# Kernel optimization log

Measured on AMD Instinct MI355X. Metric: run time of the kernel, lower is better.

Reference implementation:

```python
import jax, jax.numpy as jnp
import numpy as np

NUM_BITS = 10
D_MODEL = 256
D_INNER = 512                      # expand=2 * hidden
D_STATE = 64
N_HEADS = 8                        # D_INNER // head_dim(64)
HEAD_DIM = 64
CONV_DIM = D_INNER + 2 * D_STATE   # 640
D_PROJ = D_INNER + CONV_DIM + N_HEADS  # 1160
KERNEL = 4
EPS = 1e-5
N_TOKENS = 16384


def _hilbert_code(coords):
    # coords: (N,3) int32 in [0, 2**NUM_BITS); Skilling's AxesToTranspose + bit interleave
    n = 3
    x = [coords[:, i] for i in range(n)]
    M = 1 << (NUM_BITS - 1)
    Q = M
    while Q > 1:
        P = Q - 1
        for i in range(n):
            cond = (x[i] & Q) > 0
            t = (x[0] ^ x[i]) & P
            x0_new = jnp.where(cond, x[0] ^ P, x[0] ^ t)
            xi_new = jnp.where(cond, x[i], x[i] ^ t)
            x[0] = x0_new
            if i > 0:
                x[i] = xi_new
        Q >>= 1
    for i in range(1, n):
        x[i] = x[i] ^ x[i - 1]
    t = jnp.zeros_like(x[0])
    Q = M
    while Q > 1:
        t = jnp.where((x[n - 1] & Q) > 0, t ^ (Q - 1), t)
        Q >>= 1
    x = [xi ^ t for xi in x]
    code = jnp.zeros_like(x[0])
    for b in range(NUM_BITS - 1, -1, -1):
        for i in range(n):
            code = (code << 1) | ((x[i] >> b) & 1)
    return code


def _serialized_orders(query_pos):
    # quantize to a 2**NUM_BITS grid, Hilbert-encode, sort ('hilbert' and 'hilbert-trans' = x/y swapped)
    pmin = query_pos.min(0)
    pmax = query_pos.max(0)
    g = ((query_pos - pmin) / (pmax - pmin + 1e-6) * (2 ** NUM_BITS - 1))
    g = jnp.clip(g, 0, 2 ** NUM_BITS - 1).astype(jnp.int32)
    orders, inverses = [], []
    for perm in ((0, 1, 2), (1, 0, 2)):
        code = _hilbert_code(g[:, jnp.array(perm)])
        o = jnp.argsort(code)
        orders.append(o)
        inverses.append(jnp.argsort(o))
    return orders, inverses


def _ln(x, w, b):
    m = x.mean(-1, keepdims=True)
    xc = x - m
    return xc * jax.lax.rsqrt(jnp.mean(xc * xc, -1, keepdims=True) + EPS) * w + b


def _mamba2(x, p):
    # x: (B, L, D_MODEL)
    B, L, _ = x.shape
    zxbcdt = x @ p['in_proj']                           # (B,L,1160)
    gate = zxbcdt[..., :D_INNER]
    xBC = zxbcdt[..., D_INNER:D_INNER + CONV_DIM]
    dt = zxbcdt[..., D_INNER + CONV_DIM:]               # (B,L,H)
    # causal depthwise conv over time
    xc = jnp.moveaxis(xBC, -1, 1)                       # (B,C,L)
    xc = jax.lax.conv_general_dilated(
        xc, p['conv_w'][:, None, :], window_strides=(1,),
        padding=[(KERNEL - 1, 0)], dimension_numbers=('NCH', 'OIH', 'NCH'),
        feature_group_count=CONV_DIM)
    xc = xc + p['conv_b'][None, :, None]
    xBC = jax.nn.silu(jnp.moveaxis(xc, 1, -1))          # (B,L,C)
    xs = xBC[..., :D_INNER].reshape(B, L, N_HEADS, HEAD_DIM)
    Bm = xBC[..., D_INNER:D_INNER + D_STATE]            # (B,L,S), n_groups=1 broadcast over heads
    Cm = xBC[..., D_INNER + D_STATE:]                   # (B,L,S)
    dt = jax.nn.softplus(dt + p['dt_bias'])             # (B,L,H)
    A = -jnp.exp(p['A_log'])                            # (H,)
    dA = jnp.exp(dt * A)                                # (B,L,H)

    def step(h, inp):
        dA_t, dt_t, x_t, B_t, C_t = inp                 # (B,H),(B,H),(B,H,P),(B,S),(B,S)
        h = h * dA_t[..., None, None] + (dt_t[..., None] * x_t)[..., None] * B_t[:, None, None, :]
        y = jnp.einsum('bhps,bs->bhp', h, C_t)
        return h, y

    tm = lambda a: jnp.moveaxis(a, 1, 0)
    h0 = jnp.zeros((B, N_HEADS, HEAD_DIM, D_STATE), x.dtype)
    _, ys = jax.lax.scan(step, h0, (tm(dA), tm(dt), tm(xs), tm(Bm), tm(Cm)))
    y = jnp.moveaxis(ys, 0, 1) + p['D'][None, None, :, None] * xs   # (B,L,H,P) + D skip
    y = y.reshape(B, L, D_INNER)
    # gated RMSNorm (MambaRMSNormGated)
    y = y * jax.nn.silu(gate)
    y = y * jax.lax.rsqrt(jnp.mean(y * y, -1, keepdims=True) + EPS) * p['norm_w']
    return y @ p['out_proj']                            # (B,L,D_MODEL)


def _forward(query, query_pos, pre_w, pre_b, fin_w, fin_b, layer_params):
    orders, invs = _serialized_orders(query_pos)
    q = query
    for p in layer_params:
        shortcut = q
        qn = _ln(q, pre_w, pre_b)
        stacked = jnp.stack([qn[orders[0]], qn[orders[1]]])   # (2, N, d) multi-path serialization
        y = _mamba2(stacked, p)
        q = shortcut + (y[0][invs[0]] + y[1][invs[1]]) * 0.5  # scatter back + average paths
        q = _ln(q, fin_w, fin_b)
    return q


def setup_inputs() -> dict:
    key = jax.random.key(0)
    ks = jax.random.split(key, 24)
    inp = {
        'query': jax.random.normal(ks[0], (N_TOKENS, D_MODEL), jnp.float32),
        'query_pos': jax.random.uniform(ks[1], (N_TOKENS, 3), jnp.float32),
        'pre_w': jnp.ones((D_MODEL,), jnp.float32),
        'pre_b': jnp.zeros((D_MODEL,), jnp.float32),
        'fin_w': jnp.ones((D_MODEL,), jnp.float32),
        'fin_b': jnp.zeros((D_MODEL,), jnp.float32),
    }
    for i in range(2):
        k = jax.random.split(ks[2 + i], 6)
        inp[f'in_proj{i}'] = jax.random.normal(k[0], (D_MODEL, D_PROJ), jnp.float32) * 0.02
        inp[f'conv_w{i}'] = jax.random.normal(k[1], (CONV_DIM, KERNEL), jnp.float32) * 0.2
        inp[f'conv_b{i}'] = jnp.zeros((CONV_DIM,), jnp.float32)
        inp[f'dt_bias{i}'] = jax.random.uniform(k[2], (N_HEADS,), jnp.float32, -4.0, -1.0)
        inp[f'A_log{i}'] = jnp.log(jnp.arange(1, N_HEADS + 1, dtype=jnp.float32))
        inp[f'D{i}'] = jnp.ones((N_HEADS,), jnp.float32)
        inp[f'norm_w{i}'] = jnp.ones((D_INNER,), jnp.float32)
        inp[f'out_proj{i}'] = jax.random.normal(k[3], (D_INNER, D_MODEL), jnp.float32) * 0.02
    return inp


def reference(query, query_pos, pre_w, pre_b, fin_w, fin_b,
              in_proj0, conv_w0, conv_b0, dt_bias0, A_log0, D0, norm_w0, out_proj0,
              in_proj1, conv_w1, conv_b1, dt_bias1, A_log1, D1, norm_w1, out_proj1):
    layer_params = [
        dict(in_proj=in_proj0, conv_w=conv_w0, conv_b=conv_b0, dt_bias=dt_bias0,
             A_log=A_log0, D=D0, norm_w=norm_w0, out_proj=out_proj0),
        dict(in_proj=in_proj1, conv_w=conv_w1, conv_b=conv_b1, dt_bias=dt_bias1,
             A_log=A_log1, D=D1, norm_w=norm_w1, out_proj=out_proj1),
    ]
    return _forward(query, query_pos, pre_w, pre_b, fin_w, fin_b, layer_params)
```

## Files before the change

kernel.cpp:

```cpp
#include <hip/hip_runtime.h>
#include <stdint.h>

#define L_TOK 16384
#define DM 256
#define DI 512
#define DS 64
#define NH 8
#define HD 64
#define CD 640
#define DP 1160
#define CHUNK 64
#define NC 256
#define EPSF 1e-5f

typedef __attribute__((ext_vector_type(8))) short short8;
typedef __attribute__((ext_vector_type(4))) float f32x4;

#define GLL16(gp, lp) __builtin_amdgcn_global_load_lds((const __attribute__((address_space(1))) void*)(gp), (__attribute__((address_space(3))) void*)(lp), 16, 0, 0)

__device__ __forceinline__ float warp_sum(float v) {
  v += __shfl_xor(v, 1, 64);
  v += __shfl_xor(v, 2, 64);
  v += __shfl_xor(v, 4, 64);
  v += __shfl_xor(v, 8, 64);
  v += __shfl_xor(v, 16, 64);
  v += __shfl_xor(v, 32, 64);
  return v;
}

__device__ __forceinline__ float fexp(float x) { return __expf(x); }
__device__ __forceinline__ float fsilu(float x) { return x * __builtin_amdgcn_rcpf(1.0f + __expf(-x)); }

__device__ __forceinline__ unsigned short f2bf(float f) {
  unsigned int u = __float_as_uint(f);
  unsigned int r = (u + 0x7FFFu + ((u >> 16) & 1u)) >> 16;
  return (unsigned short)r;
}
__device__ __forceinline__ float bf2f(unsigned short u) {
  return __uint_as_float(((unsigned int)u) << 16);
}


__global__ __launch_bounds__(256) void minmax_part(const float* __restrict__ pos, float* __restrict__ part) {
  __shared__ float sm[6][4];
  int tid = threadIdx.x;
  int t = blockIdx.x*256 + tid;
  float a = pos[t*3+0], b = pos[t*3+1], c = pos[t*3+2];
  float mn0=a, mn1=b, mn2=c, mx0=a, mx1=b, mx2=c;
  #pragma unroll
  for (int d = 1; d < 64; d <<= 1) {
    mn0=fminf(mn0,__shfl_xor(mn0,d,64));
    mn1=fminf(mn1,__shfl_xor(mn1,d,64));
    mn2=fminf(mn2,__shfl_xor(mn2,d,64));
    mx0=fmaxf(mx0,__shfl_xor(mx0,d,64));
    mx1=fmaxf(mx1,__shfl_xor(mx1,d,64));
    mx2=fmaxf(mx2,__shfl_xor(mx2,d,64));
  }
  if ((tid & 63) == 0) {
    int w = tid >> 6;
    sm[0][w]=mn0; sm[1][w]=mn1; sm[2][w]=mn2;
    sm[3][w]=mx0; sm[4][w]=mx1; sm[5][w]=mx2;
  }
  __syncthreads();
  if (tid < 6) {
    float r = sm[tid][0];
    if (tid < 3) { r=fminf(r,sm[tid][1]); r=fminf(r,sm[tid][2]); r=fminf(r,sm[tid][3]); }
    else         { r=fmaxf(r,sm[tid][1]); r=fmaxf(r,sm[tid][2]); r=fmaxf(r,sm[tid][3]); }
    part[blockIdx.x*6 + tid] = r;
  }
}

__device__ unsigned int hilbert3(unsigned int a, unsigned int b, unsigned int c) {
  unsigned int x0 = a, x1 = b, x2 = c;
  for (unsigned int Q = 512u; Q > 1u; Q >>= 1) {
    unsigned int P = Q - 1u;
    { if (x0 & Q) x0 ^= P; }
    {
      unsigned int t = (x0 ^ x1) & P;
      if (x1 & Q) { x0 ^= P; }
      else { x0 ^= t; x1 ^= t; }
    }
    {
      unsigned int t = (x0 ^ x2) & P;
      if (x2 & Q) { x0 ^= P; }
      else { x0 ^= t; x2 ^= t; }
    }
  }
  x1 ^= x0; x2 ^= x1;
  unsigned int tt = 0;
  for (unsigned int Q = 512u; Q > 1u; Q >>= 1)
    if (x2 & Q) tt ^= (Q - 1u);
  x0 ^= tt; x1 ^= tt; x2 ^= tt;
  unsigned int code = 0;
  #pragma unroll
  for (int bb = 9; bb >= 0; --bb) {
    code = (code << 1) | ((x0 >> bb) & 1u);
    code = (code << 1) | ((x1 >> bb) & 1u);
    code = (code << 1) | ((x2 >> bb) & 1u);
  }
  return code;
}

__global__ __launch_bounds__(256) void hilbert_kernel(const float* __restrict__ pos, const float* __restrict__ part,
                                                      unsigned long long* __restrict__ keys) {
  __shared__ float spmm[6];
  int tid = threadIdx.x;
  if (tid < 64) {
    const float* p = part + tid*6;
    float mn0=p[0], mn1=p[1], mn2=p[2], mx0=p[3], mx1=p[4], mx2=p[5];
    #pragma unroll
    for (int d = 1; d < 64; d <<= 1) {
      mn0=fminf(mn0,__shfl_xor(mn0,d,64));
      mn1=fminf(mn1,__shfl_xor(mn1,d,64));
      mn2=fminf(mn2,__shfl_xor(mn2,d,64));
      mx0=fmaxf(mx0,__shfl_xor(mx0,d,64));
      mx1=fmaxf(mx1,__shfl_xor(mx1,d,64));
      mx2=fmaxf(mx2,__shfl_xor(mx2,d,64));
    }
    if (tid == 0) {
      spmm[0]=mn0; spmm[1]=mn1; spmm[2]=mn2;
      spmm[3]=mx0; spmm[4]=mx1; spmm[5]=mx2;
    }
  }
  __syncthreads();
  int t = blockIdx.x*256 + tid;
  unsigned int g[3];
  #pragma unroll
  for (int d = 0; d < 3; ++d) {
    float v = (pos[t*3+d] - spmm[d]) / (spmm[3+d] - spmm[d] + 1e-6f) * 1023.0f;
    v = fminf(fmaxf(v, 0.0f), 1023.0f);
    g[d] = (unsigned int)(int)v;
  }
  unsigned int ca = hilbert3(g[0], g[1], g[2]);
  unsigned int cb = hilbert3(g[1], g[0], g[2]);
  keys[t]         = ((unsigned long long)ca << 14) | (unsigned long long)t;
  keys[L_TOK + t] = ((unsigned long long)cb << 14) | (unsigned long long)t;
}

__global__ __launch_bounds__(256) void sort_tiles(const unsigned long long* __restrict__ keys,
                                                  unsigned long long* __restrict__ skeys) {
  __shared__ unsigned long long s[512];
  int b = blockIdx.x, tid = threadIdx.x;
  size_t base = (size_t)(b >> 5)*L_TOK + (size_t)(b & 31)*512;
  s[tid]       = keys[base + tid];
  s[tid + 256] = keys[base + tid + 256];
  for (unsigned int k = 2; k <= 512; k <<= 1) {
    for (unsigned int j = k >> 1; j > 0; j >>= 1) {
      __syncthreads();
      #pragma unroll
      for (int h = 0; h < 2; ++h) {
        int i = tid + 256*h;
        int ixj = i ^ (int)j;
        if (ixj > i) {
          unsigned long long a = s[i], c = s[ixj];
          bool up = ((i & (int)k) == 0);
          if (up ? (a > c) : (a < c)) { s[i] = c; s[ixj] = a; }
        }
      }
    }
  }
  __syncthreads();
  skeys[base + tid]       = s[tid];
  skeys[base + tid + 256] = s[tid + 256];
}

__global__ __launch_bounds__(256) void rank_partial(const unsigned long long* __restrict__ keys,
                                                    const unsigned long long* __restrict__ skeys,
                                                    unsigned int* __restrict__ partial) {
  __shared__ unsigned long long tile[512];
  int arr = blockIdx.y, ks = blockIdx.z;
  const unsigned long long* k = keys + (size_t)arr * L_TOK;
  int qbase = blockIdx.x*1024 + threadIdx.x;
  unsigned long long q[4];
  #pragma unroll
  for (int i = 0; i < 4; ++i) q[i] = k[qbase + 256*i];
  const unsigned long long* src = skeys + (size_t)arr*L_TOK + ks*512;
  tile[threadIdx.x]       = src[threadIdx.x];
  tile[threadIdx.x + 256] = src[threadIdx.x + 256];
  __syncthreads();
  #pragma unroll
  for (int i = 0; i < 4; ++i) {
    unsigned int lo = 0;
    #pragma unroll
    for (unsigned int st = 256; st > 0; st >>= 1)
      if (tile[lo + st - 1] < q[i]) lo += st;
    lo += (tile[lo] < q[i]) ? 1u : 0u;
    partial[(size_t)(ks*2 + arr)*L_TOK + qbase + 256*i] = lo;
  }
}

__global__ __launch_bounds__(256) void rank_scatter(const unsigned long long* __restrict__ keys,
                                                    const unsigned int* __restrict__ partial,
                                                    unsigned int* __restrict__ ord,
                                                    unsigned int* __restrict__ inv) {
  int i = blockIdx.x*256 + threadIdx.x;
  int arr = i >> 14;
  int qi = i & (L_TOK - 1);
  unsigned int r = 0;
  #pragma unroll
  for (int ks = 0; ks < 32; ++ks) r += partial[(size_t)(ks*2 + arr)*L_TOK + qi];
  unsigned int tok = (unsigned int)(keys[i] & 0x3FFFu);
  ord[(size_t)arr*L_TOK + r] = tok;
  inv[(size_t)arr*L_TOK + tok] = r;
}


__global__ __launch_bounds__(256) void ln_kernel(const float* __restrict__ in, float* __restrict__ out,
                                                 unsigned short* __restrict__ outbf,
                                                 const float* __restrict__ w, const float* __restrict__ b) {
  int row = blockIdx.x*4 + (threadIdx.x >> 6);
  int lane = threadIdx.x & 63;
  const float4 v = *(const float4*)(in + (size_t)row*DM + lane*4);
  float s = v.x + v.y + v.z + v.w;
  float mean = warp_sum(s) * (1.0f/DM);
  float4 xc = make_float4(v.x-mean, v.y-mean, v.z-mean, v.w-mean);
  float ss = xc.x*xc.x + xc.y*xc.y + xc.z*xc.z + xc.w*xc.w;
  ss = warp_sum(ss) * (1.0f/DM);
  float inv = rsqrtf(ss + EPSF);
  const float4 w4 = *(const float4*)(w + lane*4);
  const float4 b4 = *(const float4*)(b + lane*4);
  float4 o;
  o.x = xc.x*inv*w4.x + b4.x;
  o.y = xc.y*inv*w4.y + b4.y;
  o.z = xc.z*inv*w4.z + b4.z;
  o.w = xc.w*inv*w4.w + b4.w;
  *(float4*)(out + (size_t)row*DM + lane*4) = o;
  if (outbf) {
    ushort4 ob = make_ushort4(f2bf(o.x), f2bf(o.y), f2bf(o.z), f2bf(o.w));
    *(ushort4*)(outbf + (size_t)row*DM + lane*4) = ob;
  }
}

__global__ __launch_bounds__(256) void lnfuse_kernel(float* __restrict__ io,
                                                     float* __restrict__ qn, unsigned short* __restrict__ qnbf,
                                                     const float* __restrict__ fw, const float* __restrict__ fb,
                                                     const float* __restrict__ pw, const float* __restrict__ pb) {
  int row = blockIdx.x*4 + (threadIdx.x >> 6);
  int lane = threadIdx.x & 63;
  const float4 v = *(const float4*)(io + (size_t)row*DM + lane*4);
  float s = v.x + v.y + v.z + v.w;
  float mean = warp_sum(s) * (1.0f/DM);
  float4 xc = make_float4(v.x-mean, v.y-mean, v.z-mean, v.w-mean);
  float ss = xc.x*xc.x + xc.y*xc.y + xc.z*xc.z + xc.w*xc.w;
  ss = warp_sum(ss) * (1.0f/DM);
  float inv = rsqrtf(ss + EPSF);
  const float4 w4 = *(const float4*)(fw + lane*4);
  const float4 b4 = *(const float4*)(fb + lane*4);
  float4 o;
  o.x = xc.x*inv*w4.x + b4.x;
  o.y = xc.y*inv*w4.y + b4.y;
  o.z = xc.z*inv*w4.z + b4.z;
  o.w = xc.w*inv*w4.w + b4.w;
  *(float4*)(io + (size_t)row*DM + lane*4) = o;
  if (qn) {
    float s2 = o.x + o.y + o.z + o.w;
    float mean2 = warp_sum(s2) * (1.0f/DM);
    float4 x2 = make_float4(o.x-mean2, o.y-mean2, o.z-mean2, o.w-mean2);
    float ss2 = x2.x*x2.x + x2.y*x2.y + x2.z*x2.z + x2.w*x2.w;
    ss2 = warp_sum(ss2) * (1.0f/DM);
    float inv2 = rsqrtf(ss2 + EPSF);
    const float4 pw4 = *(const float4*)(pw + lane*4);
    const float4 pb4 = *(const float4*)(pb + lane*4);
    float4 qv;
    qv.x = x2.x*inv2*pw4.x + pb4.x;
    qv.y = x2.y*inv2*pw4.y + pb4.y;
    qv.z = x2.z*inv2*pw4.z + pb4.z;
    qv.w = x2.w*inv2*pw4.w + pb4.w;
    *(float4*)(qn + (size_t)row*DM + lane*4) = qv;
    ushort4 qb = make_ushort4(f2bf(qv.x), f2bf(qv.y), f2bf(qv.z), f2bf(qv.w));
    *(ushort4*)(qnbf + (size_t)row*DM + lane*4) = qb;
  }
}


__global__ __launch_bounds__(256) void tcvt_both(const float* __restrict__ Wi, const float* __restrict__ Wo,
                                                 const float* __restrict__ nw,
                                                 unsigned short* __restrict__ WtA, unsigned short* __restrict__ WtO) {
  __shared__ float lds[64*65];
  int b = blockIdx.x, tid = threadIdx.x;
  const float* src; int srcld, n0, k0t, dstld; unsigned short* dst; bool useNw;
  if (b < 72) {
    int nt = b >> 2, kt = b & 3;
    n0 = nt*64; k0t = kt*64;
    src = Wi; srcld = DP; dst = WtA; dstld = 256; useNw = false;
  } else {
    int j = b - 72;
    int nt = j >> 3, kt = j & 7;
    n0 = nt*64; k0t = kt*64;
    src = Wo; srcld = DM; dst = WtO; dstld = 512; useNw = true;
  }
  int nn = (tid & 15)*4, kk = tid >> 4;
  #pragma unroll
  for (int p = 0; p < 4; ++p) {
    int k = kk + p*16;
    float4 v = *(const float4*)(src + (size_t)(k0t + k)*srcld + n0 + nn);
    lds[k*65 + nn]   = v.x;
    lds[k*65 + nn+1] = v.y;
    lds[k*65 + nn+2] = v.z;
    lds[k*65 + nn+3] = v.w;
  }
  __syncthreads();
  int n = tid >> 2, kq = (tid & 3)*16;
  float nwv[16];
  if (useNw) {
    #pragma unroll
    for (int e = 0; e < 16; e += 4) {
      float4 t4 = *(const float4*)(nw + k0t + kq + e);
      nwv[e]=t4.x; nwv[e+1]=t4.y; nwv[e+2]=t4.z; nwv[e+3]=t4.w;
    }
  } else {
    #pragma unroll
    for (int e = 0; e < 16; ++e) nwv[e] = 1.0f;
  }
  short8 o0, o1;
  #pragma unroll
  for (int e = 0; e < 8; ++e) {
    o0[e] = (short)f2bf(lds[(kq+e)*65 + n] * nwv[e]);
    o1[e] = (short)f2bf(lds[(kq+8+e)*65 + n] * nwv[8+e]);
  }
  unsigned short* dp = dst + (size_t)(n0 + n)*dstld + k0t + kq;
  *(short8*)dp = o0;
  *(short8*)(dp + 8) = o1;
}


__global__ __launch_bounds__(256) void gemm_in2(const unsigned short* __restrict__ Abf,
                                                const unsigned short* __restrict__ Wt,
                                                const unsigned int* __restrict__ ord,
                                                unsigned short* __restrict__ gate_nat,
                                                unsigned short* __restrict__ bcraw,
                                                unsigned short* __restrict__ xTg) {
  __shared__ unsigned short Alds[128*64];
  __shared__ unsigned short Blds[128*64];
  int tid = threadIdx.x, lane = tid & 63, w = tid >> 6;
  int bid = blockIdx.x;
  bool natp = bid < 640;
  int rb, cb, dir = 0, wcol0;
  if (natp) {
    int xcd = bid & 7, g = bid >> 3;
    rb = (xcd*16 + g/5)*128;
    cb = (g % 5)*128;
    wcol0 = cb;
  } else {
    int id = bid - 640;
    dir = id >> 9;
    int b = id & 511;
    int xcd = b & 7, g = b >> 3;
    rb = (xcd*16 + g/4)*128;
    cb = (g % 4)*128;
    wcol0 = DI + cb;
  }
  int wm = (w & 1)*64, wn = (w >> 1)*64;
  const unsigned int* ordp = ord + (size_t)dir*L_TOK;
  const unsigned short* pA[4]; const unsigned short* pB[4];
  unsigned short* dA[4]; unsigned short* dB[4];
  #pragma unroll
  for (int s = 0; s < 4; ++s) {
    int inst = w*4 + s;
    int r = inst*8 + (lane >> 3);
    int cA = (lane & 7) ^ (r & 7);
    int arow = natp ? (rb + r) : (int)ordp[rb + r];
    pA[s] = Abf + (size_t)arow*DM + cA*8;
    pB[s] = Wt + (size_t)(wcol0 + r)*DM + cA*8;
    dA[s] = &Alds[inst*512];
    dB[s] = &Blds[inst*512];
  }
  f32x4 zero = {0.f, 0.f, 0.f, 0.f};
  f32x4 acc[4][4];
  #pragma unroll
  for (int i = 0; i < 4; ++i)
    #pragma unroll
    for (int j = 0; j < 4; ++j) acc[i][j] = zero;
  int t = lane & 15, q = lane >> 4;
  for (int k0 = 0; k0 < DM; k0 += 64) {
    #pragma unroll
    for (int s = 0; s < 4; ++s) GLL16(pA[s] + k0, dA[s]);
    #pragma unroll
    for (int s = 0; s < 4; ++s) GLL16(pB[s] + k0, dB[s]);
    __syncthreads();
    #pragma unroll
    for (int ks = 0; ks < 2; ++ks) {
      short8 af[4], bfr[4];
      int cc = ks*4 + q;
      #pragma unroll
      for (int i = 0; i < 4; ++i) {
        int rr = wm + 16*i + t;
        af[i] = *(const short8*)&Alds[rr*64 + ((cc ^ (rr & 7))*8)];
      }
      #pragma unroll
      for (int j = 0; j < 4; ++j) {
        int rr = wn + 16*j + t;
        bfr[j] = *(const short8*)&Blds[rr*64 + ((cc ^ (rr & 7))*8)];
      }
      #pragma unroll
      for (int i = 0; i < 4; ++i)
        #pragma unroll
        for (int j = 0; j < 4; ++j)
          acc[i][j] = __builtin_amdgcn_mfma_f32_16x16x32_bf16(af[i], bfr[j], acc[i][j], 0, 0, 0);
    }
    __syncthreads();
  }
  if (natp) {
    unsigned short* dst; int ld;
    if (cb < DI) { dst = gate_nat + cb; ld = DI; }
    else         { dst = bcraw + (cb - DI); ld = 128; }
    #pragma unroll
    for (int i = 0; i < 4; ++i) {
      int rowb = rb + wm + 16*i + q*4;
      #pragma unroll
      for (int j = 0; j < 4; ++j) {
        int col = wn + 16*j + t;
        #pragma unroll
        for (int r = 0; r < 4; ++r)
          dst[(size_t)(rowb + r)*ld + col] = f2bf(acc[i][j][r]);
      }
    }
  } else {
    #pragma unroll
    for (int i = 0; i < 4; ++i) {
      int rowb = rb + wm + 16*i + q*4;
      #pragma unroll
      for (int j = 0; j < 4; ++j) {
        int col = wn + 16*j + t;
        ushort4 o = make_ushort4(f2bf(acc[i][j][0]), f2bf(acc[i][j][1]),
                                 f2bf(acc[i][j][2]), f2bf(acc[i][j][3]));
        *(ushort4*)(xTg + (size_t)(cb + col)*(2*L_TOK) + (size_t)dir*L_TOK + rowb) = o;
      }
    }
  }
}


__global__ __launch_bounds__(256) void gemm_out_gather(const unsigned short* __restrict__ ybuf,
                                                       const unsigned short* __restrict__ Wt,
                                                       const unsigned int* __restrict__ inv,
                                                       const float* __restrict__ rms_acc,
                                                       const float* __restrict__ shortcut,
                                                       float* __restrict__ out) {
  __shared__ unsigned short Alds[2*64*64];
  __shared__ unsigned short Blds[128*64];
  int tid = threadIdx.x, lane = tid & 63, w = tid >> 6;
  int bid = blockIdx.x;
  int xcd = bid & 7, g = bid >> 3;
  int rb = (xcd*32 + (g >> 1))*64;
  int cb = (g & 1)*128;
  int wm = (w & 1)*32, wn = (w >> 1)*64;
  const unsigned short* pA0[2]; const unsigned short* pA1[2];
  unsigned short* dA0[2]; unsigned short* dA1[2];
  const unsigned short* pB[4]; unsigned short* dB[4];
  #pragma unroll
  for (int s = 0; s < 2; ++s) {
    int inst = w*2 + s;
    int r = inst*8 + (lane >> 3);
    int cA = (lane & 7) ^ (r & 7);
    int tok = rb + r;
    pA0[s] = ybuf + (size_t)inv[tok]*DI + cA*8;
    pA1[s] = ybuf + (size_t)L_TOK*DI + (size_t)inv[L_TOK + tok]*DI + cA*8;
    dA0[s] = &Alds[inst*512];
    dA1[s] = &Alds[4096 + inst*512];
  }
  #pragma unroll
  for (int s = 0; s < 4; ++s) {
    int inst = w*4 + s;
    int r = inst*8 + (lane >> 3);
    int cA = (lane & 7) ^ (r & 7);
    pB[s] = Wt + (size_t)(cb + r)*DI + cA*8;
    dB[s] = &Blds[inst*512];
  }
  f32x4 zero = {0.f, 0.f, 0.f, 0.f};
  f32x4 acc0[2][4], acc1[2][4];
  #pragma unroll
  for (int i = 0; i < 2; ++i)
    #pragma unroll
    for (int j = 0; j < 4; ++j) { acc0[i][j] = zero; acc1[i][j] = zero; }
  int t = lane & 15, q = lane >> 4;
  for (int k0 = 0; k0 < DI; k0 += 64) {
    #pragma unroll
    for (int s = 0; s < 2; ++s) { GLL16(pA0[s] + k0, dA0[s]); GLL16(pA1[s] + k0, dA1[s]); }
    #pragma unroll
    for (int s = 0; s < 4; ++s) GLL16(pB[s] + k0, dB[s]);
    __syncthreads();
    #pragma unroll
    for (int ks = 0; ks < 2; ++ks) {
      short8 af0[2], af1[2], bfr[4];
      int cc = ks*4 + q;
      #pragma unroll
      for (int i = 0; i < 2; ++i) {
        int rr = wm + 16*i + t;
        int off = rr*64 + ((cc ^ (rr & 7))*8);
        af0[i] = *(const short8*)&Alds[off];
        af1[i] = *(const short8*)&Alds[4096 + off];
      }
      #pragma unroll
      for (int j = 0; j < 4; ++j) {
        int rr = wn + 16*j + t;
        bfr[j] = *(const short8*)&Blds[rr*64 + ((cc ^ (rr & 7))*8)];
      }
      #pragma unroll
      for (int i = 0; i < 2; ++i)
        #pragma unroll
        for (int j = 0; j < 4; ++j) {
          acc0[i][j] = __builtin_amdgcn_mfma_f32_16x16x32_bf16(af0[i], bfr[j], acc0[i][j], 0, 0, 0);
          acc1[i][j] = __builtin_amdgcn_mfma_f32_16x16x32_bf16(af1[i], bfr[j], acc1[i][j], 0, 0, 0);
        }
    }
    __syncthreads();
  }
  #pragma unroll
  for (int i = 0; i < 2; ++i) {
    #pragma unroll
    for (int r = 0; r < 4; ++r) {
      int row = rb + wm + 16*i + q*4 + r;
      float ir0 = rsqrtf(rms_acc[row]*(1.0f/DI) + EPSF);
      float ir1 = rsqrtf(rms_acc[L_TOK + row]*(1.0f/DI) + EPSF);
      const float* sp = shortcut + (size_t)row*DM + cb;
      float* op = out + (size_t)row*DM + cb;
      #pragma unroll
      for (int j = 0; j < 4; ++j) {
        int col = wn + 16*j + t;
        op[col] = sp[col] + 0.5f*(ir0*acc0[i][j][r] + ir1*acc1[i][j][r]);
      }
    }
  }
}


__global__ __launch_bounds__(256) void dtconv(const float* __restrict__ qn, const float* __restrict__ W,
                                              const float* __restrict__ dt_bias, float* __restrict__ dtb,
                                              float* __restrict__ rms_acc,
                                              const unsigned short* __restrict__ bcraw,
                                              const float* __restrict__ cw, const float* __restrict__ cbias,
                                              const unsigned int* __restrict__ ord,
                                              unsigned short* __restrict__ bcswz,
                                              unsigned short* __restrict__ bcswzA) {
  __shared__ unsigned short smem[131*64];
  int tid = threadIdx.x;
  int bx = blockIdx.x;
  if (bx < 512) {
    int gid = bx*256 + tid;
    if (gid < 2*L_TOK) rms_acc[gid] = 0.f;
    float* Wl = (float*)smem;
    {
      const float* wp = W + (size_t)tid*DP + (DI + CD);
      float4 wa = *(const float4*)wp;
      float4 wb = *(const float4*)(wp + 4);
      int off = tid*8 + (tid >> 5)*4;
      *(float4*)&Wl[off]     = wa;
      *(float4*)&Wl[off + 4] = wb;
    }
    __syncthreads();
    int lane = tid & 63, w = tid >> 6;
    int r = bx*32 + w*8 + (lane >> 3);
    int kg = lane & 7;
    const float* qp = qn + (size_t)r*DM + kg*32;
    float acc[8] = {};
    #pragma unroll
    for (int i = 0; i < 8; ++i) {
      float4 q4 = *(const float4*)(qp + i*4);
      float qv[4] = {q4.x, q4.y, q4.z, q4.w};
      #pragma unroll
      for (int e = 0; e < 4; ++e) {
        int k = kg*32 + i*4 + e;
        int off = k*8 + kg*4;
        float4 wa = *(const float4*)&Wl[off];
        float4 wb = *(const float4*)&Wl[off + 4];
        acc[0] = fmaf(qv[e], wa.x, acc[0]);
        acc[1] = fmaf(qv[e], wa.y, acc[1]);
        acc[2] = fmaf(qv[e], wa.z, acc[2]);
        acc[3] = fmaf(qv[e], wa.w, acc[3]);
        acc[4] = fmaf(qv[e], wb.x, acc[4]);
        acc[5] = fmaf(qv[e], wb.y, acc[5]);
        acc[6] = fmaf(qv[e], wb.z, acc[6]);
        acc[7] = fmaf(qv[e], wb.w, acc[7]);
      }
    }
    #pragma unroll
    for (int h = 0; h < 8; ++h) {
      acc[h] += __shfl_xor(acc[h], 8, 64);
      acc[h] += __shfl_xor(acc[h], 16, 64);
      acc[h] += __shfl_xor(acc[h], 32, 64);
    }
    float v = 0.f;
    #pragma unroll
    for (int h = 0; h < 8; ++h) if (kg == h) v = acc[h];
    v += dt_bias[kg];
    float sp = (v > 0.0f) ? (v + log1pf(__expf(-v))) : log1pf(__expf(v));
    dtb[(size_t)r*NH + kg] = sp;
  } else {
    int cid = bx - 512;
    int half = cid & 1, ty = (cid >> 1) & 127, dir = cid >> 8;
    unsigned short* tile = smem;
    const unsigned int* ordp = ord + (size_t)dir*L_TOK;
    int ch0 = DI + half*64;
    int co0 = half*64;
    int t0 = ty*128;
    for (int cc = tid; cc < 131*8; cc += 256) {
      int r = cc >> 3, cgc = cc & 7;
      int t = t0 - 3 + r;
      short8 v = {0,0,0,0,0,0,0,0};
      if (t >= 0) v = *(const short8*)(bcraw + (size_t)ordp[t]*128 + co0 + cgc*8);
      *(short8*)&tile[r*64 + ((cgc ^ (r & 7))*8)] = v;
    }
    int cg = tid & 7, tp = tid >> 3;
    int ch = ch0 + cg*8;
    float wv[8][4];
    float bias[8];
    #pragma unroll
    for (int e = 0; e < 8; ++e) {
      float4 c4 = *(const float4*)(cw + (ch + e)*4);
      wv[e][0] = c4.x; wv[e][1] = c4.y; wv[e][2] = c4.z; wv[e][3] = c4.w;
    }
    {
      float4 b0 = *(const float4*)(cbias + ch);
      float4 b1 = *(const float4*)(cbias + ch + 4);
      bias[0]=b0.x; bias[1]=b0.y; bias[2]=b0.z; bias[3]=b0.w;
      bias[4]=b1.x; bias[5]=b1.y; bias[6]=b1.z; bias[7]=b1.w;
    }
    __syncthreads();
    #pragma unroll
    for (int tk = 0; tk < 4; ++tk) {
      int rel = tp + 32*tk;
      float acc[8];
      #pragma unroll
      for (int e = 0; e < 8; ++e) acc[e] = bias[e];
      #pragma unroll
      for (int k = 0; k < 4; ++k) {
        int r = rel + k;
        short8 v = *(const short8*)&tile[r*64 + ((cg ^ (r & 7))*8)];
        #pragma unroll
        for (int e = 0; e < 8; ++e)
          acc[e] = fmaf(wv[e][k], bf2f((unsigned short)v[e]), acc[e]);
      }
      short8 o;
      #pragma unroll
      for (int e = 0; e < 8; ++e) o[e] = (short)f2bf(fsilu(acc[e]));
      int T = t0 + rel;
      int chn = T >> 6, tl = T & 63;
      unsigned short* tb = bcswz + ((size_t)((dir*NC + chn)*2 + half))*4096;
      *(short8*)(tb + tl*64 + ((cg ^ (tl & 7))*8)) = o;
      if (half == 0) {
        unsigned short* ta = bcswzA + ((size_t)(dir*NC + chn))*4096;
        #pragma unroll
        for (int e = 0; e < 8; ++e) {
          int s5 = cg*8 + e;
          ta[s5*64 + (((tl >> 3) ^ (s5 & 7))*8) + (tl & 7)] = (unsigned short)o[e];
        }
      }
    }
  }
}


__global__ __launch_bounds__(256) void phaseA_mfma(const unsigned short* __restrict__ xTg,
                                                   const unsigned short* __restrict__ bcswzA,
                                                   const float* __restrict__ cw, const float* __restrict__ cbias,
                                                   const float* __restrict__ dtb, const float* __restrict__ A_log,
                                                   const unsigned int* __restrict__ ord,
                                                   unsigned short* __restrict__ S, float* __restrict__ P,
                                                   unsigned short* __restrict__ xsT) {
  int c = blockIdx.x, h = blockIdx.y, dir = blockIdx.z, tid = threadIdx.x;
  int lane = tid & 63, w = tid >> 6;
  int hh = dir*NH + h;
  __shared__ unsigned short xT[64*64];
  __shared__ unsigned short Bt[64*64];
  __shared__ float wgt[64];
  int c0 = c*CHUNK;
  float Ah = -expf(A_log[h]);
  const unsigned short* bA = bcswzA + ((size_t)(dir*NC + c))*4096;
  #pragma unroll
  for (int s = 0; s < 2; ++s) {
    int inst = w*2 + s;
    GLL16(bA + (size_t)inst*512 + lane*8, &Bt[inst*512]);
  }
  if (tid < 64) {
    unsigned int tok = ord[(size_t)dir*L_TOK + c0 + tid];
    float dtv = dtb[(size_t)tok*NH + h];
    float v = dtv*Ah;
    float s = v;
    #pragma unroll
    for (int d = 1; d < 64; d <<= 1) {
      float u = __shfl_down(s, d, 64);
      s += (tid + d < 64) ? u : 0.f;
    }
    wgt[tid] = dtv*fexp(s - v);
    if (tid == 0) P[hh*NC + c] = fexp(s);
  }
  __syncthreads();
  unsigned short* xpg = xsT + ((size_t)(hh*NC + c))*4096;
  #pragma unroll
  for (int i = 0; i < 2; ++i) {
    int q = tid + 256*i;
    int p = q >> 3, tg = q & 7;
    int sw8 = (tg ^ (p & 7))*8;
    const unsigned short* xrow = xTg + (size_t)(h*HD + p)*(2*L_TOK) + (size_t)dir*L_TOK;
    int tb = c0 + tg*8;
    short8 cur = *(const short8*)(xrow + tb);
    int sh5 = __shfl_up((int)(unsigned short)cur[5], 1, 64);
    int sh6 = __shfl_up((int)(unsigned short)cur[6], 1, 64);
    int sh7 = __shfl_up((int)(unsigned short)cur[7], 1, 64);
    unsigned short b5 = 0, b6 = 0, b7 = 0;
    if (tg == 0) {
      if (tb >= 8) {
        ushort4 pv = *(const ushort4*)(xrow + tb - 4);
        b5 = pv.y; b6 = pv.z; b7 = pv.w;
      }
    } else {
      b5 = (unsigned short)sh5; b6 = (unsigned short)sh6; b7 = (unsigned short)sh7;
    }
    float4 w4 = *(const float4*)(cw + (size_t)(h*HD + p)*4);
    float bb = cbias[h*HD + p];
    float xv[11];
    xv[0] = bf2f(b5);
    xv[1] = bf2f(b6);
    xv[2] = bf2f(b7);
    #pragma unroll
    for (int k = 0; k < 8; ++k) xv[3+k] = bf2f((unsigned short)cur[k]);
    short8 raw, wtd;
    #pragma unroll
    for (int k = 0; k < 8; ++k) {
      float a = bb + w4.x*xv[k] + w4.y*xv[k+1] + w4.z*xv[k+2] + w4.w*xv[k+3];
      unsigned short rbf = f2bf(fsilu(a));
      raw[k] = (short)rbf;
      wtd[k] = (short)f2bf(bf2f(rbf)*wgt[tg*8 + k]);
    }
    *(short8*)(xpg + p*64 + sw8) = raw;
    *(short8*)&xT[p*64 + sw8] = wtd;
  }
  __syncthreads();
  int t16 = lane & 15, q4 = lane >> 4;
  f32x4 zero = {0.f,0.f,0.f,0.f};
  f32x4 acc[4];
  #pragma unroll
  for (int j = 0; j < 4; ++j) acc[j] = zero;
  #pragma unroll
  for (int ks = 0; ks < 2; ++ks) {
    int rowA = 16*w + t16;
    short8 a = *(const short8*)&xT[rowA*64 + (((ks*4 + q4) ^ (rowA & 7))*8)];
    #pragma unroll
    for (int j = 0; j < 4; ++j) {
      int rowB = 16*j + t16;
      short8 b = *(const short8*)&Bt[rowB*64 + (((ks*4 + q4) ^ (rowB & 7))*8)];
      acc[j] = __builtin_amdgcn_mfma_f32_16x16x32_bf16(a, b, acc[j], 0, 0, 0);
    }
  }
  unsigned short* Sp = S + ((size_t)(hh*NC + c))*4096;
  #pragma unroll
  for (int j = 0; j < 4; ++j)
    #pragma unroll
    for (int r = 0; r < 4; ++r) {
      int row = 16*w + q4*4 + r;
      int cg2 = 2*j + (t16 >> 3);
      Sp[(size_t)row*64 + (((cg2 ^ (row & 7)) << 3) | (t16 & 7))] = f2bf(acc[j][r]);
    }
}


__global__ __launch_bounds__(128) void phaseB_scan(unsigned short* __restrict__ S, const float* __restrict__ P) {
  __shared__ float Pl[NC];
  int b = blockIdx.x;
  int hh = b >> 4;
  int e2 = (b & 15)*128 + threadIdx.x;
  for (int i = threadIdx.x; i < NC; i += 128) Pl[i] = P[hh*NC + i];
  __syncthreads();
  unsigned int* base = (unsigned int*)(S + ((size_t)hh*NC)*4096) + e2;
  float hx = 0.f, hy = 0.f;
  #pragma unroll 1
  for (int k0 = 0; k0 < NC; k0 += 16) {
    unsigned int v[16];
    #pragma unroll
    for (int u = 0; u < 16; ++u) v[u] = base[(size_t)(k0+u)*2048];
    #pragma unroll
    for (int u = 0; u < 16; ++u) {
      float p = Pl[k0+u];
      unsigned int old = v[u];
      base[(size_t)(k0+u)*2048] = (unsigned int)f2bf(hx) | ((unsigned int)f2bf(hy) << 16);
      hx = p*hx + bf2f((unsigned short)(old & 0xffffu));
      hy = p*hy + bf2f((unsigned short)(old >> 16));
    }
  }
}

__global__ __launch_bounds__(256) void phaseC_mfma(const unsigned short* __restrict__ bcswz,
                                                   const unsigned short* __restrict__ xsT,
                                                   const unsigned short* __restrict__ gate_nat,
                                                   const float* __restrict__ dtb, const float* __restrict__ A_log,
                                                   const float* __restrict__ Dp,
                                                   const unsigned int* __restrict__ ord,
                                                   const unsigned short* __restrict__ S,
                                                   unsigned short* __restrict__ ybuf,
                                                   float* __restrict__ rms_acc) {
  int c = blockIdx.x, h = blockIdx.y, dir = blockIdx.z, tid = threadIdx.x;
  int lane = tid & 63, w = tid >> 6;
  int hh = dir*NH + h;
  unsigned short* y = ybuf + (size_t)dir*L_TOK*DI;
  __shared__ __align__(16) unsigned short smemT[4*4096];
  __shared__ float dts[64], pl[64], pe[64];
  unsigned short* Cl  = smemT;
  unsigned short* Bl  = smemT + 4096;
  unsigned short* h0l = smemT + 8192;
  unsigned short* xT  = smemT + 12288;
  float* fT = (float*)(smemT + 8192);
  int c0 = c*CHUNK;
  float Ah = -expf(A_log[h]);
  float Dh = Dp[h];
  const unsigned short* Sp = S + ((size_t)(hh*NC + c))*4096;
  const unsigned short* xp = xsT + ((size_t)(hh*NC + c))*4096;
  const unsigned short* Bg = bcswz + ((size_t)((dir*NC + c)*2 + 0))*4096;
  const unsigned short* Cg = bcswz + ((size_t)((dir*NC + c)*2 + 1))*4096;
  #pragma unroll
  for (int s = 0; s < 2; ++s) {
    int inst = w*2 + s;
    GLL16(Sp + (size_t)inst*512 + lane*8, &h0l[inst*512]);
    GLL16(xp + (size_t)inst*512 + lane*8, &xT[inst*512]);
    GLL16(Bg + (size_t)inst*512 + lane*8, &Bl[inst*512]);
    GLL16(Cg + (size_t)inst*512 + lane*8, &Cl[inst*512]);
  }
  int erow = tid >> 2;
  int ech0 = (tid & 3) * 16;
  unsigned int etok = ord[(size_t)dir*L_TOK + c0 + erow];
  const unsigned short* gp = gate_nat + (size_t)etok*DI + h*HD + ech0;
  short8 g0 = *(const short8*)gp;
  short8 g1 = *(const short8*)(gp + 8);
  if (tid < 64) {
    unsigned int tok = ord[(size_t)dir*L_TOK + c0 + tid];
    float dtv = dtb[(size_t)tok*NH + h];
    dts[tid] = dtv;
    float v = dtv*Ah;
    float s = v;
    #pragma unroll
    for (int d = 1; d < 64; d <<= 1) {
      float u = __shfl_up(s, d, 64);
      s += (tid >= d) ? u : 0.f;
    }
    pl[tid] = s;
    pe[tid] = fexp(s);
  }
  __syncthreads();
  int t16 = lane & 15, q4 = lane >> 4;
  int t0 = 16*w;
  f32x4 zero = {0.f,0.f,0.f,0.f};
  f32x4 accG[4], accY[4];
  #pragma unroll
  for (int j = 0; j < 4; ++j) { accG[j] = zero; accY[j] = zero; }
  #pragma unroll
  for (int ks = 0; ks < 2; ++ks) {
    int rowA = t0 + t16;
    short8 a = *(const short8*)&Cl[rowA*64 + (((ks*4 + q4) ^ (rowA & 7))*8)];
    #pragma unroll
    for (int j = 0; j < 4; ++j) {
      int rowB = 16*j + t16;
      int off = rowB*64 + (((ks*4 + q4) ^ (rowB & 7))*8);
      accG[j] = __builtin_amdgcn_mfma_f32_16x16x32_bf16(a, *(const short8*)&Bl[off], accG[j], 0, 0, 0);
      accY[j] = __builtin_amdgcn_mfma_f32_16x16x32_bf16(a, *(const short8*)&h0l[off], accY[j], 0, 0, 0);
    }
  }
  #pragma unroll
  for (int j = 0; j < 4; ++j) {
    #pragma unroll
    for (int r = 0; r < 4; ++r) {
      int t = t0 + q4*4 + r;
      int s = 16*j + t16;
      float v = 0.f;
      if (s <= t) {
        v = accG[j][r] * dts[s] * fexp(pl[t] - pl[s]);
        if (s == t) v += Dh;
      }
      Cl[t*64 + (((s >> 3) ^ (t & 7))*8 + (s & 7))] = f2bf(v);
    }
  }
  #pragma unroll
  for (int j = 0; j < 4; ++j)
    #pragma unroll
    for (int r = 0; r < 4; ++r)
      accY[j][r] *= pe[t0 + q4*4 + r];
  #pragma unroll
  for (int ks = 0; ks < 2; ++ks) {
    int rowA = t0 + t16;
    short8 a = *(const short8*)&Cl[rowA*64 + (((ks*4 + q4) ^ (rowA & 7))*8)];
    #pragma unroll
    for (int j = 0; j < 4; ++j) {
      int rowB = 16*j + t16;
      short8 b = *(const short8*)&xT[rowB*64 + (((ks*4 + q4) ^ (rowB & 7))*8)];
      accY[j] = __builtin_amdgcn_mfma_f32_16x16x32_bf16(a, b, accY[j], 0, 0, 0);
    }
  }
  __syncthreads();
  #pragma unroll
  for (int j = 0; j < 4; ++j)
    #pragma unroll
    for (int r = 0; r < 4; ++r) {
      int t = t0 + q4*4 + r;
      int p = 16*j + t16;
      fT[t*64 + (p ^ (q4 << 4))] = accY[j][r];
    }
  __syncthreads();
  {
    int swz = ((erow >> 2) & 3) << 4;
    const float* fr = &fT[erow*64 + (ech0 ^ swz)];
    float4 a0 = *(const float4*)(fr);
    float4 a1 = *(const float4*)(fr + 4);
    float4 a2 = *(const float4*)(fr + 8);
    float4 a3 = *(const float4*)(fr + 12);
    float fv[16] = {a0.x,a0.y,a0.z,a0.w, a1.x,a1.y,a1.z,a1.w,
                    a2.x,a2.y,a2.z,a2.w, a3.x,a3.y,a3.z,a3.w};
    float sq = 0.f;
    short8 o0, o1;
    #pragma unroll
    for (int e = 0; e < 8; ++e) {
      float v0 = fv[e]   * fsilu(bf2f((unsigned short)g0[e]));
      float v1 = fv[8+e] * fsilu(bf2f((unsigned short)g1[e]));
      o0[e] = (short)f2bf(v0);
      o1[e] = (short)f2bf(v1);
      sq += v0*v0 + v1*v1;
    }
    unsigned short* yp = y + (size_t)(c0 + erow)*DI + h*HD + ech0;
    *(short8*)yp = o0;
    *(short8*)(yp + 8) = o1;
    sq += __shfl_xor(sq, 1, 64);
    sq += __shfl_xor(sq, 2, 64);
    if ((tid & 3) == 0) atomicAdd(&rms_acc[(size_t)dir*L_TOK + etok], sq);
  }
}

__global__ void fill_debug(float* out, float v) {
  int i = blockIdx.x*256 + threadIdx.x;
  if (i < L_TOK*DM) out[i] = v;
}


extern "C" void kernel_launch(void* const* d_in, const int* in_sizes, int n_in,
                              void* d_out, int out_size, void* d_ws, size_t ws_size,
                              hipStream_t stream) {
  const float* query = (const float*)d_in[0];
  const float* qpos  = (const float*)d_in[1];
  const float* pre_w = (const float*)d_in[2];
  const float* pre_b = (const float*)d_in[3];
  const float* fin_w = (const float*)d_in[4];
  const float* fin_b = (const float*)d_in[5];
  float* out = (float*)d_out;

  char* ws = (char*)d_ws;
  size_t off = 0;
  auto alloc = [&](size_t bytes) -> void* {
    void* p = ws + off;
    off += (bytes + 255) & ~(size_t)255;
    return p;
  };
  unsigned long long* keys = (unsigned long long*)alloc((size_t)2*L_TOK*8);
  unsigned long long* skeys = (unsigned long long*)alloc((size_t)2*L_TOK*8);
  unsigned int* ord = (unsigned int*)alloc((size_t)2*L_TOK*4);
  unsigned int* inv = (unsigned int*)alloc((size_t)2*L_TOK*4);
  unsigned int* rpart = (unsigned int*)alloc((size_t)32*2*L_TOK*4);
  float* mmpart = (float*)alloc((size_t)64*6*4);
  float* qn   = (float*)alloc((size_t)L_TOK*DM*4);
  unsigned short* qnbf = (unsigned short*)alloc((size_t)L_TOK*DM*2);
  unsigned short* gate_nat = (unsigned short*)alloc((size_t)L_TOK*DI*2);
  unsigned short* xTg    = (unsigned short*)alloc((size_t)512*2*L_TOK*2);
  unsigned short* bcraw  = (unsigned short*)alloc((size_t)L_TOK*128*2);
  unsigned short* bcswz  = (unsigned short*)alloc((size_t)2*NC*2*4096*2);
  unsigned short* bcswzA = (unsigned short*)alloc((size_t)2*NC*4096*2);
  unsigned short* ybuf   = (unsigned short*)alloc((size_t)2*L_TOK*DI*2);
  float* dtb  = (float*)alloc((size_t)L_TOK*NH*4);
  float* rms_acc = (float*)alloc((size_t)2*L_TOK*4);
  unsigned short* Sbuf = (unsigned short*)alloc((size_t)2*NH*NC*4096*2);
  unsigned short* xsT  = (unsigned short*)alloc((size_t)2*NH*NC*4096*2);
  float* Pbuf = (float*)alloc((size_t)2*NH*NC*4);
  unsigned short* WtA = (unsigned short*)alloc((size_t)1152*DM*2);
  unsigned short* WtO = (unsigned short*)alloc((size_t)DM*DI*2);
  if (off > ws_size) {
    fill_debug<<<(L_TOK*DM + 255)/256, 256, 0, stream>>>(out, (float)(ws_size >> 20));
    return;
  }

  minmax_part<<<64, 256, 0, stream>>>(qpos, mmpart);
  hilbert_kernel<<<L_TOK/256, 256, 0, stream>>>(qpos, mmpart, keys);
  sort_tiles<<<64, 256, 0, stream>>>(keys, skeys);
  rank_partial<<<dim3(16, 2, 32), 256, 0, stream>>>(keys, skeys, rpart);
  rank_scatter<<<(2*L_TOK)/256, 256, 0, stream>>>(keys, rpart, ord, inv);

  for (int l = 0; l < 2; ++l) {
    int base = 6 + 8*l;
    const float* in_proj  = (const float*)d_in[base+0];
    const float* conv_w   = (const float*)d_in[base+1];
    const float* conv_b   = (const float*)d_in[base+2];
    const float* dt_bias  = (const float*)d_in[base+3];
    const float* A_log    = (const float*)d_in[base+4];
    const float* Dp       = (const float*)d_in[base+5];
    const float* norm_w   = (const float*)d_in[base+6];
    const float* out_proj = (const float*)d_in[base+7];

    if (l == 0)
      ln_kernel<<<L_TOK/4, 256, 0, stream>>>(query, qn, qnbf, pre_w, pre_b);
    tcvt_both<<<104, 256, 0, stream>>>(in_proj, out_proj, norm_w, WtA, WtO);
    gemm_in2<<<1664, 256, 0, stream>>>(qnbf, WtA, ord, gate_nat, bcraw, xTg);
    dtconv<<<1024, 256, 0, stream>>>(qn, in_proj, dt_bias, dtb, rms_acc,
                                     bcraw, conv_w, conv_b, ord, bcswz, bcswzA);
    phaseA_mfma<<<dim3(NC, NH, 2), 256, 0, stream>>>(xTg, bcswzA, conv_w, conv_b, dtb, A_log, ord, Sbuf, Pbuf, xsT);
    phaseB_scan<<<256, 128, 0, stream>>>(Sbuf, Pbuf);
    phaseC_mfma<<<dim3(NC, NH, 2), 256, 0, stream>>>(bcswz, xsT, gate_nat, dtb, A_log, Dp, ord, Sbuf, ybuf, rms_acc);
    gemm_out_gather<<<512, 256, 0, stream>>>(ybuf, WtO, inv, rms_acc,
                                             l ? (const float*)out : query, out);
    if (l == 0)
      lnfuse_kernel<<<L_TOK/4, 256, 0, stream>>>(out, qn, qnbf, fin_w, fin_b, pre_w, pre_b);
    else
      lnfuse_kernel<<<L_TOK/4, 256, 0, stream>>>(out, nullptr, nullptr, fin_w, fin_b, pre_w, pre_b);
  }
}
```

Baseline: 444.4 us.

## Compute RMS sums inside out-projection GEMM, batch weight conversion, reorder chunk grid

Removes the atomicAdd-based per-token RMS accumulation in phaseC and the zeroing pass in dtconv. Instead, the out-projection GEMM squares the bf16 A fragments it already loads from LDS and reduces them per row. Both layers' weight transpose/convert run in a single launch before the layer loop. The phaseA/phaseC grid is also swapped so heads vary fastest. This trades global atomics and an extra buffer for some extra ALU work in two of the GEMM waves. The norm is now computed from bf16-rounded y rather than fp32, a small precision difference.

Result: no change. 452.4 us (+1.8%).

```diff
diff --git a/kernel.cpp b/kernel.cpp
--- a/kernel.cpp
+++ b/kernel.cpp
@@ -273,11 +273,20 @@
 }
 
 
-__global__ __launch_bounds__(256) void tcvt_both(const float* __restrict__ Wi, const float* __restrict__ Wo,
-                                                 const float* __restrict__ nw,
-                                                 unsigned short* __restrict__ WtA, unsigned short* __restrict__ WtO) {
+__global__ __launch_bounds__(256) void tcvt_all(const float* __restrict__ Wi0, const float* __restrict__ Wo0,
+                                                const float* __restrict__ nw0,
+                                                const float* __restrict__ Wi1, const float* __restrict__ Wo1,
+                                                const float* __restrict__ nw1,
+                                                unsigned short* __restrict__ WtA, unsigned short* __restrict__ WtO) {
   __shared__ float lds[64*65];
   int b = blockIdx.x, tid = threadIdx.x;
+  int lyr = (b >= 104) ? 1 : 0;
+  b -= lyr*104;
+  const float* Wi = lyr ? Wi1 : Wi0;
+  const float* Wo = lyr ? Wo1 : Wo0;
+  const float* nw = lyr ? nw1 : nw0;
+  WtA += (size_t)lyr*1152*DM;
+  WtO += (size_t)lyr*DM*DI;
   const float* src; int srcld, n0, k0t, dstld; unsigned short* dst; bool useNw;
   if (b < 72) {
     int nt = b >> 2, kt = b & 3;
@@ -434,17 +443,18 @@
 __global__ __launch_bounds__(256) void gemm_out_gather(const unsigned short* __restrict__ ybuf,
                                                        const unsigned short* __restrict__ Wt,
                                                        const unsigned int* __restrict__ inv,
-                                                       const float* __restrict__ rms_acc,
                                                        const float* __restrict__ shortcut,
                                                        float* __restrict__ out) {
   __shared__ unsigned short Alds[2*64*64];
   __shared__ unsigned short Blds[128*64];
+  __shared__ float sql[2][64];
   int tid = threadIdx.x, lane = tid & 63, w = tid >> 6;
   int bid = blockIdx.x;
   int xcd = bid & 7, g = bid >> 3;
   int rb = (xcd*32 + (g >> 1))*64;
   int cb = (g & 1)*128;
   int wm = (w & 1)*32, wn = (w >> 1)*64;
+  bool rmsw = ((w >> 1) == 0);
   const unsigned short* pA0[2]; const unsigned short* pA1[2];
   unsigned short* dA0[2]; unsigned short* dA1[2];
   const unsigned short* pB[4]; unsigned short* dB[4];
@@ -473,6 +483,7 @@
   for (int i = 0; i < 2; ++i)
     #pragma unroll
     for (int j = 0; j < 4; ++j) { acc0[i][j] = zero; acc1[i][j] = zero; }
+  float sq0[2] = {0.f, 0.f}, sq1[2] = {0.f, 0.f};
   int t = lane & 15, q = lane >> 4;
   for (int k0 = 0; k0 < DI; k0 += 64) {
     #pragma unroll
@@ -490,6 +501,17 @@
         int off = rr*64 + ((cc ^ (rr & 7))*8);
         af0[i] = *(const short8*)&Alds[off];
         af1[i] = *(const short8*)&Alds[4096 + off];
+      }
+      if (rmsw) {
+        #pragma unroll
+        for (int i = 0; i < 2; ++i)
+          #pragma unroll
+          for (int e = 0; e < 8; ++e) {
+            float a0 = bf2f((unsigned short)af0[i][e]);
+            float a1 = bf2f((unsigned short)af1[i][e]);
+            sq0[i] = fmaf(a0, a0, sq0[i]);
+            sq1[i] = fmaf(a1, a1, sq1[i]);
+          }
       }
       #pragma unroll
       for (int j = 0; j < 4; ++j) {
@@ -506,13 +528,27 @@
     }
     __syncthreads();
   }
+  if (rmsw) {
+    #pragma unroll
+    for (int i = 0; i < 2; ++i) {
+      float s0 = sq0[i];
+      s0 += __shfl_xor(s0, 16, 64);
+      s0 += __shfl_xor(s0, 32, 64);
+      float s1 = sq1[i];
+      s1 += __shfl_xor(s1, 16, 64);
+      s1 += __shfl_xor(s1, 32, 64);
+      if (q == 0) { sql[0][wm + 16*i + t] = s0; sql[1][wm + 16*i + t] = s1; }
+    }
+  }
+  __syncthreads();
   #pragma unroll
   for (int i = 0; i < 2; ++i) {
     #pragma unroll
     for (int r = 0; r < 4; ++r) {
-      int row = rb + wm + 16*i + q*4 + r;
-      float ir0 = rsqrtf(rms_acc[row]*(1.0f/DI) + EPSF);
-      float ir1 = rsqrtf(rms_acc[L_TOK + row]*(1.0f/DI) + EPSF);
+      int rl = wm + 16*i + q*4 + r;
+      int row = rb + rl;
+      float ir0 = rsqrtf(sql[0][rl]*(1.0f/DI) + EPSF);
+      float ir1 = rsqrtf(sql[1][rl]*(1.0f/DI) + EPSF);
       const float* sp = shortcut + (size_t)row*DM + cb;
       float* op = out + (size_t)row*DM + cb;
       #pragma unroll
@@ -527,7 +563,6 @@
 
 __global__ __launch_bounds__(256) void dtconv(const float* __restrict__ qn, const float* __restrict__ W,
                                               const float* __restrict__ dt_bias, float* __restrict__ dtb,
-                                              float* __restrict__ rms_acc,
                                               const unsigned short* __restrict__ bcraw,
                                               const float* __restrict__ cw, const float* __restrict__ cbias,
                                               const unsigned int* __restrict__ ord,
@@ -537,8 +572,6 @@
   int tid = threadIdx.x;
   int bx = blockIdx.x;
   if (bx < 512) {
-    int gid = bx*256 + tid;
-    if (gid < 2*L_TOK) rms_acc[gid] = 0.f;
     float* Wl = (float*)smem;
     {
       const float* wp = W + (size_t)tid*DP + (DI + CD);
@@ -658,7 +691,7 @@
                                                    const unsigned int* __restrict__ ord,
                                                    unsigned short* __restrict__ S, float* __restrict__ P,
                                                    unsigned short* __restrict__ xsT) {
-  int c = blockIdx.x, h = blockIdx.y, dir = blockIdx.z, tid = threadIdx.x;
+  int h = blockIdx.x, c = blockIdx.y, dir = blockIdx.z, tid = threadIdx.x;
   int lane = tid & 63, w = tid >> 6;
   int hh = dir*NH + h;
   __shared__ unsigned short xT[64*64];
@@ -787,9 +820,8 @@
                                                    const float* __restrict__ Dp,
                                                    const unsigned int* __restrict__ ord,
                                                    const unsigned short* __restrict__ S,
-                                                   unsigned short* __restrict__ ybuf,
-                                                   float* __restrict__ rms_acc) {
-  int c = blockIdx.x, h = blockIdx.y, dir = blockIdx.z, tid = threadIdx.x;
+                                                   unsigned short* __restrict__ ybuf) {
+  int h = blockIdx.x, c = blockIdx.y, dir = blockIdx.z, tid = threadIdx.x;
   int lane = tid & 63, w = tid >> 6;
   int hh = dir*NH + h;
   unsigned short* y = ybuf + (size_t)dir*L_TOK*DI;
@@ -903,7 +935,6 @@
     float4 a3 = *(const float4*)(fr + 12);
     float fv[16] = {a0.x,a0.y,a0.z,a0.w, a1.x,a1.y,a1.z,a1.w,
                     a2.x,a2.y,a2.z,a2.w, a3.x,a3.y,a3.z,a3.w};
-    float sq = 0.f;
     short8 o0, o1;
     #pragma unroll
     for (int e = 0; e < 8; ++e) {
@@ -911,14 +942,10 @@
       float v1 = fv[8+e] * fsilu(bf2f((unsigned short)g1[e]));
       o0[e] = (short)f2bf(v0);
       o1[e] = (short)f2bf(v1);
-      sq += v0*v0 + v1*v1;
     }
     unsigned short* yp = y + (size_t)(c0 + erow)*DI + h*HD + ech0;
     *(short8*)yp = o0;
     *(short8*)(yp + 8) = o1;
-    sq += __shfl_xor(sq, 1, 64);
-    sq += __shfl_xor(sq, 2, 64);
-    if ((tid & 3) == 0) atomicAdd(&rms_acc[(size_t)dir*L_TOK + etok], sq);
   }
 }
 
@@ -961,12 +988,11 @@
   unsigned short* bcswzA = (unsigned short*)alloc((size_t)2*NC*4096*2);
   unsigned short* ybuf   = (unsigned short*)alloc((size_t)2*L_TOK*DI*2);
   float* dtb  = (float*)alloc((size_t)L_TOK*NH*4);
-  float* rms_acc = (float*)alloc((size_t)2*L_TOK*4);
   unsigned short* Sbuf = (unsigned short*)alloc((size_t)2*NH*NC*4096*2);
   unsigned short* xsT  = (unsigned short*)alloc((size_t)2*NH*NC*4096*2);
   float* Pbuf = (float*)alloc((size_t)2*NH*NC*4);
-  unsigned short* WtA = (unsigned short*)alloc((size_t)1152*DM*2);
-  unsigned short* WtO = (unsigned short*)alloc((size_t)DM*DI*2);
+  unsigned short* WtA = (unsigned short*)alloc((size_t)2*1152*DM*2);
+  unsigned short* WtO = (unsigned short*)alloc((size_t)2*DM*DI*2);
   if (off > ws_size) {
     fill_debug<<<(L_TOK*DM + 255)/256, 256, 0, stream>>>(out, (float)(ws_size >> 20));
     return;
@@ -977,6 +1003,9 @@
   sort_tiles<<<64, 256, 0, stream>>>(keys, skeys);
   rank_partial<<<dim3(16, 2, 32), 256, 0, stream>>>(keys, skeys, rpart);
   rank_scatter<<<(2*L_TOK)/256, 256, 0, stream>>>(keys, rpart, ord, inv);
+  tcvt_all<<<208, 256, 0, stream>>>((const float*)d_in[6], (const float*)d_in[13], (const float*)d_in[12],
+                                    (const float*)d_in[14], (const float*)d_in[21], (const float*)d_in[20],
+                                    WtA, WtO);
 
   for (int l = 0; l < 2; ++l) {
     int base = 6 + 8*l;
@@ -986,19 +1015,18 @@
     const float* dt_bias  = (const float*)d_in[base+3];
     const float* A_log    = (const float*)d_in[base+4];
     const float* Dp       = (const float*)d_in[base+5];
-    const float* norm_w   = (const float*)d_in[base+6];
-    const float* out_proj = (const float*)d_in[base+7];
+    const unsigned short* WtAl = WtA + (size_t)l*1152*DM;
+    const unsigned short* WtOl = WtO + (size_t)l*DM*DI;
 
     if (l == 0)
       ln_kernel<<<L_TOK/4, 256, 0, stream>>>(query, qn, qnbf, pre_w, pre_b);
-    tcvt_both<<<104, 256, 0, stream>>>(in_proj, out_proj, norm_w, WtA, WtO);
-    gemm_in2<<<1664, 256, 0, stream>>>(qnbf, WtA, ord, gate_nat, bcraw, xTg);
-    dtconv<<<1024, 256, 0, stream>>>(qn, in_proj, dt_bias, dtb, rms_acc,
+    gemm_in2<<<1664, 256, 0, stream>>>(qnbf, WtAl, ord, gate_nat, bcraw, xTg);
+    dtconv<<<1024, 256, 0, stream>>>(qn, in_proj, dt_bias, dtb,
                                      bcraw, conv_w, conv_b, ord, bcswz, bcswzA);
-    phaseA_mfma<<<dim3(NC, NH, 2), 256, 0, stream>>>(xTg, bcswzA, conv_w, conv_b, dtb, A_log, ord, Sbuf, Pbuf, xsT);
+    phaseA_mfma<<<dim3(NH, NC, 2), 256, 0, stream>>>(xTg, bcswzA, conv_w, conv_b, dtb, A_log, ord, Sbuf, Pbuf, xsT);
     phaseB_scan<<<256, 128, 0, stream>>>(Sbuf, Pbuf);
-    phaseC_mfma<<<dim3(NC, NH, 2), 256, 0, stream>>>(bcswz, xsT, gate_nat, dtb, A_log, Dp, ord, Sbuf, ybuf, rms_acc);
-    gemm_out_gather<<<512, 256, 0, stream>>>(ybuf, WtO, inv, rms_acc,
+    phaseC_mfma<<<dim3(NH, NC, 2), 256, 0, stream>>>(bcswz, xsT, gate_nat, dtb, A_log, Dp, ord, Sbuf, ybuf);
+    gemm_out_gather<<<512, 256, 0, stream>>>(ybuf, WtOl, inv,
                                              l ? (const float*)out : query, out);
     if (l == 0)
       lnfuse_kernel<<<L_TOK/4, 256, 0, stream>>>(out, qn, qnbf, fin_w, fin_b, pre_w, pre_b);
```
